# Kernel tuning notes

Measured on AMD Instinct MI355X. Metric: run time of the kernel, lower is better.

## Reference

```python
import jax, jax.numpy as jnp
import numpy as np

SF = 2  # shrink_factor


def resize_bilinear_ac(x, oh, ow):
    """Bilinear resize with align_corners=True, NCHW, matches torch F.interpolate."""
    B, C, H, W = x.shape
    if (oh, ow) == (H, W):
        return x
    ys = jnp.linspace(0.0, H - 1, oh)
    y0 = jnp.floor(ys).astype(jnp.int32)
    y1 = jnp.clip(y0 + 1, 0, H - 1)
    wy = (ys - y0).astype(x.dtype)
    xs = jnp.linspace(0.0, W - 1, ow)
    x0 = jnp.floor(xs).astype(jnp.int32)
    x1 = jnp.clip(x0 + 1, 0, W - 1)
    wx = (xs - x0).astype(x.dtype)
    t = x[:, :, y0, :] * (1 - wy)[None, None, :, None] + x[:, :, y1, :] * wy[None, None, :, None]
    return t[:, :, :, x0] * (1 - wx) + t[:, :, :, x1] * wx


def conv1x1(x, W, b):
    # x: [B,C,H,W], W: [O,C], b: [O]
    return jnp.einsum('bchw,oc->bohw', x, W) + b[None, :, None, None]


def setup_inputs() -> dict:
    key = jax.random.key(0)
    ks = jax.random.split(key, 8)
    B, C, H, W = 4, 512, 129, 129
    Cqk = C // 8
    s = 1.0 / np.sqrt(C)
    return {
        'x': jax.random.normal(ks[0], (B, C, H, W), jnp.float32),
        'Wq': jax.random.normal(ks[1], (Cqk, C), jnp.float32) * s,
        'bq': jax.random.normal(ks[2], (Cqk,), jnp.float32) * s,
        'Wk': jax.random.normal(ks[3], (Cqk, C), jnp.float32) * s,
        'bk': jax.random.normal(ks[4], (Cqk,), jnp.float32) * s,
        'Wv': jax.random.normal(ks[5], (C, C), jnp.float32) * s,
        'bv': jax.random.normal(ks[6], (C,), jnp.float32) * s,
        'gamma': jax.random.normal(ks[7], (1,), jnp.float32) * 0.1,
    }


def reference(x, Wq, bq, Wk, bk, Wv, bv, gamma):
    B, C, H, W = x.shape
    h = (H - 1) // SF + 1
    w = (W - 1) // SF + 1
    xs = resize_bilinear_ac(x, h, w)  # [B,C,h,w]
    N = h * w
    q = conv1x1(xs, Wq, bq).reshape(B, -1, N)  # [B,Cqk,N]
    k = conv1x1(xs, Wk, bk).reshape(B, -1, N)  # [B,Cqk,N]
    v = conv1x1(xs, Wv, bv).reshape(B, -1, N)  # [B,C,N]
    # energy[b,n,m] = <q[:,n], k[:,m]>
    energy = jnp.einsum('bcn,bcm->bnm', q, k)  # [B,N,N]
    attention = jax.nn.softmax(energy, axis=-1)
    # out[b,c,n] = sum_m v[b,c,m] * attention[b,n,m]  (bmm(value, attention^T))
    out = jnp.einsum('bcm,bnm->bcn', v, attention).reshape(B, C, h, w)
    Hu = (h - 1) * SF + 1
    Wu = (w - 1) * SF + 1
    out = resize_bilinear_ac(out, Hu, Wu)
    out = gamma[0] * out + x
    return out, energy
```

## Files before the change

### kernel.cpp

```cpp
#include <hip/hip_runtime.h>
#include <hip/hip_bf16.h>
#include <cstdint>

#define BB 4
#define CC 512
#define CQK 64
#define HH 129
#define WW 129
#define HS 65
#define WSZ 65
#define NN 4225
#define NP 4352
#define KPV 4288
#define OUTSZ 34080768
#define ESZ 17850625
#define PLANE 16641

typedef unsigned short u16;
typedef __attribute__((ext_vector_type(8))) __bf16 bfrag;
typedef __attribute__((ext_vector_type(4))) float f4v;

__device__ inline u16 f2bf(float f) {
    union { float f; unsigned int u; } v; v.f = f;
    unsigned int u = v.u;
    return (u16)((u + 0x7FFFu + ((u >> 16) & 1u)) >> 16);
}
__device__ inline float bf2f(u16 v) {
    union { unsigned u; float f; } x; x.u = (unsigned)v << 16; return x.f;
}

__device__ __forceinline__ void gload16(const u16* g, u16* l) {
    __builtin_amdgcn_global_load_lds(
        (const __attribute__((address_space(1))) void*)g,
        (__attribute__((address_space(3))) void*)l, 16, 0, 0);
}

__global__ __launch_bounds__(256) void setup_k(const float* __restrict__ Wq,
                                               const float* __restrict__ Wk,
                                               const float* __restrict__ Wv,
                                               const float* __restrict__ x,
                                               u16* __restrict__ Wc,
                                               u16* __restrict__ XsT) {
    __shared__ u16 tile[64][65];
    if (blockIdx.x < 1280) {
        int idx = blockIdx.x * 256 + threadIdx.x;
        int o = idx >> 9, c = idx & 511;
        float v = (o < 64) ? Wq[o * 512 + c] : (o < 128) ? Wk[(o - 64) * 512 + c] : Wv[(o - 128) * 512 + c];
        Wc[idx] = f2bf(v);
        return;
    }
    int bid = blockIdx.x - 1280;
    int nt = bid % 68;
    int ct = (bid / 68) & 7;
    int b = bid / 544;
    int t = threadIdx.x;
#pragma unroll
    for (int l = 0; l < 16; ++l) {
        int e = t + l * 256;
        int ci = e >> 6, nj = e & 63;
        int n = nt * 64 + nj;
        int nc = n < (NN - 1) ? n : (NN - 1);
        int i = nc / 65, j = nc % 65;
        int c = ct * 64 + ci;
        float v = x[(((size_t)b * CC + c) * HH + 2 * i) * WW + 2 * j];
        tile[ci][nj] = f2bf(v);
    }
    __syncthreads();
#pragma unroll
    for (int l = 0; l < 16; ++l) {
        int e = t + l * 256;
        int nj = e >> 6, ci = e & 63;
        XsT[((size_t)b * NP + nt * 64 + nj) * 512 + ct * 64 + ci] = tile[ci][nj];
    }
}

template <int MODE>
__global__ __launch_bounds__(256) void gemm_nt(const u16* __restrict__ Abase,
                                               const u16* __restrict__ Bbase,
                                               int K, int lda, int ldb,
                                               float* __restrict__ outF,
                                               u16* __restrict__ out1, u16* __restrict__ out2,
                                               const float* __restrict__ bq,
                                               const float* __restrict__ bk,
                                               const float* __restrict__ bv,
                                               float* __restrict__ psums) {
    __shared__ __align__(16) u16 S[16384];
    u16* As = S;
    u16* Bs = S + 8192;

    int z; size_t m0, n0; unsigned xsave = 0;
    if (MODE == 0) {
        unsigned flat = blockIdx.x;
        unsigned s = flat & 7u;
        unsigned k = flat >> 3;
        unsigned m = k % 5u;
        unsigned nl = k / 5u;
        z = (int)(s >> 1);
        m0 = (size_t)m * 128;
        n0 = ((size_t)(s & 1u) * 17u + nl) * 128;
    } else {
        z = blockIdx.z;
        m0 = (size_t)blockIdx.y * 128;
        n0 = (size_t)blockIdx.x * 128;
        xsave = blockIdx.x;
    }

    const u16* A; const u16* Bm;
    if (MODE == 0) { A = Abase;                          Bm = Bbase + (size_t)z * NP * 512; }
    if (MODE == 1) { A = Abase + (size_t)z * NP * 128;   Bm = Bbase + (size_t)z * NP * 128 + 64; }

    const u16* Ab = A + m0 * lda;
    const u16* Bb = Bm + n0 * ldb;

    const int tid = threadIdx.x;
    const int lane = tid & 63, w = tid >> 6;
    const int wr = w >> 1, wc = w & 1;
    const int frow = lane & 15, fk = (lane >> 4) * 8;

    f4v acc[4][4];
#pragma unroll
    for (int i = 0; i < 4; ++i)
#pragma unroll
        for (int j = 0; j < 4; ++j) acc[i][j] = (f4v){0.f, 0.f, 0.f, 0.f};

    for (int kt = 0; kt < K; kt += 64) {
        if (kt) __syncthreads();
#pragma unroll
        for (int it = 0; it < 4; ++it) {
            int cb = (it * 4 + w) * 64;
            int chunk = cb + lane;
            int r = chunk >> 3;
            int kc = (chunk & 7) << 3;
            gload16(Ab + (size_t)r * lda + kt + kc, &As[cb * 8]);
            gload16(Bb + (size_t)r * ldb + kt + kc, &Bs[cb * 8]);
        }
        __syncthreads();
#pragma unroll
        for (int ks = 0; ks < 2; ++ks) {
            bfrag af[4], bf[4];
#pragma unroll
            for (int i = 0; i < 4; ++i)
                af[i] = *(const bfrag*)&As[(wr * 64 + i * 16 + frow) * 64 + ks * 32 + fk];
#pragma unroll
            for (int j = 0; j < 4; ++j)
                bf[j] = *(const bfrag*)&Bs[(wc * 64 + j * 16 + frow) * 64 + ks * 32 + fk];
#pragma unroll
            for (int i = 0; i < 4; ++i)
#pragma unroll
                for (int j = 0; j < 4; ++j)
                    acc[i][j] = __builtin_amdgcn_mfma_f32_16x16x32_bf16(af[i], bf[j], acc[i][j], 0, 0, 0);
        }
    }

    const int rbase = (lane >> 4) * 4, cbase = lane & 15;

    if (MODE == 0) {
        u16* out1b = out1 + (size_t)z * NP * 128;
        u16* out2b = out2 + (size_t)z * 512 * NP;
#pragma unroll
        for (int i = 0; i < 4; ++i)
#pragma unroll
            for (int j = 0; j < 4; ++j) {
                size_t row0 = m0 + wr * 64 + i * 16 + rbase;
                size_t col = n0 + wc * 64 + j * 16 + cbase;
#pragma unroll
                for (int r = 0; r < 4; ++r) {
                    int o = (int)(row0 + r);
                    float bias = (o < 64) ? bq[o] : (o < 128) ? bk[o - 64] : bv[o - 128];
                    u16 bb = f2bf(acc[i][j][r] + bias);
                    if (o < 128) out1b[col * 128 + o] = bb;
                    else out2b[(size_t)(o - 128) * NP + col] = bb;
                }
            }
    } else {
        float* eb = outF + (size_t)z * ESZ;
        u16* Pb = out1 + (size_t)z * NP * NP;
        float psl[4][4];
#pragma unroll
        for (int i = 0; i < 4; ++i)
#pragma unroll
            for (int r = 0; r < 4; ++r) psl[i][r] = 0.f;

        __syncthreads();
#pragma unroll
        for (int i = 0; i < 4; ++i)
#pragma unroll
            for (int j = 0; j < 4; ++j) {
                int rl = wr * 64 + i * 16 + rbase;
                int cl = wc * 64 + j * 16 + cbase;
                size_t row0 = m0 + rl;
                size_t col = n0 + cl;
#pragma unroll
                for (int r = 0; r < 4; ++r) {
                    float v = acc[i][j][r];
                    size_t ro = row0 + r;
                    float pe = (col < NN) ? __expf(v) : 0.f;
                    if (ro < NN && col < NN) eb[ro * NN + col] = v;
                    S[(rl + r) * 128 + cl] = f2bf(pe);
                    psl[i][r] += pe;
                }
            }
        float* pbase = psums + ((size_t)z * 68 + xsave * 2 + wc) * NP;
#pragma unroll
        for (int i = 0; i < 4; ++i)
#pragma unroll
            for (int r = 0; r < 4; ++r) {
                float s = psl[i][r];
                s += __shfl_xor(s, 1);
                s += __shfl_xor(s, 2);
                s += __shfl_xor(s, 4);
                s += __shfl_xor(s, 8);
                if (cbase == 0)
                    pbase[m0 + wr * 64 + i * 16 + rbase + r] = s;
            }
        __syncthreads();
        u16* pb = Pb + m0 * NP + n0;
#pragma unroll
        for (int l = 0; l < 8; ++l) {
            int idx = tid + l * 256;
            int row = idx >> 4, c16 = idx & 15;
            *(int4*)(pb + (size_t)row * NP + c16 * 8) = *(const int4*)&S[row * 128 + c16 * 8];
        }
    }
}

__global__ __launch_bounds__(256) void reduce_sums(const float* __restrict__ psums,
                                                   float* __restrict__ invsum) {
    int idx = blockIdx.x * 256 + threadIdx.x;
    if (idx >= BB * NP) return;
    int b = idx / NP, n = idx % NP;
    const float* p = psums + (size_t)b * 68 * NP + n;
    float s = 0.f;
#pragma unroll
    for (int ct = 0; ct < 68; ++ct) s += p[(size_t)ct * NP];
    invsum[idx] = 1.f / s;
}

__global__ __launch_bounds__(256) void gemm_pv(const u16* __restrict__ Vb,
                                               const u16* __restrict__ P,
                                               u16* __restrict__ ctxp,
                                               const float* __restrict__ invsum) {
    __shared__ __align__(16) u16 S[16384];
    u16* As = S;
    u16* Bs = S + 8192;

    unsigned flat = blockIdx.x + 34u * (blockIdx.y + 4u * blockIdx.z);
    unsigned swz = (flat & 7u) * 136u + (flat >> 3);
    unsigned zs = swz / 136u;
    unsigned rem = swz - zs * 136u;
    unsigned xs = rem >> 2;
    unsigned ys = rem & 3u;
    const int b = (int)(zs >> 1), half = (int)(zs & 1);

    const u16* A = Vb + (size_t)b * 512 * NP;
    const u16* Bm = P + (size_t)b * NP * NP;
    const size_t m0 = (size_t)ys * 128;
    const size_t n0 = (size_t)xs * 128;
    const u16* Ab = A + m0 * NP;
    const u16* Bb = Bm + n0 * NP;
    const int kbeg = half ? 2176 : 0;
    const int kend = half ? KPV : 2176;

    const int tid = threadIdx.x;
    const int lane = tid & 63, w = tid >> 6;
    const int wr = w >> 1, wc = w & 1;
    const int frow = lane & 15, fk = (lane >> 4) * 8;

    f4v acc[4][4];
#pragma unroll
    for (int i = 0; i < 4; ++i)
#pragma unroll
        for (int j = 0; j < 4; ++j) acc[i][j] = (f4v){0.f, 0.f, 0.f, 0.f};

    for (int kt = kbeg; kt < kend; kt += 64) {
        if (kt != kbeg) __syncthreads();
#pragma unroll
        for (int it = 0; it < 4; ++it) {
            int cb = (it * 4 + w) * 64;
            int chunk = cb + lane;
            int r = chunk >> 3;
            int kc = (chunk & 7) << 3;
            gload16(Ab + (size_t)r * NP + kt + kc, &As[cb * 8]);
            gload16(Bb + (size_t)r * NP + kt + kc, &Bs[cb * 8]);
        }
        __syncthreads();
#pragma unroll
        for (int ks = 0; ks < 2; ++ks) {
            bfrag af[4], bf[4];
#pragma unroll
            for (int i = 0; i < 4; ++i)
                af[i] = *(const bfrag*)&As[(wr * 64 + i * 16 + frow) * 64 + ks * 32 + fk];
#pragma unroll
            for (int j = 0; j < 4; ++j)
                bf[j] = *(const bfrag*)&Bs[(wc * 64 + j * 16 + frow) * 64 + ks * 32 + fk];
#pragma unroll
            for (int i = 0; i < 4; ++i)
#pragma unroll
                for (int j = 0; j < 4; ++j)
                    acc[i][j] = __builtin_amdgcn_mfma_f32_16x16x32_bf16(af[i], bf[j], acc[i][j], 0, 0, 0);
        }
    }

    const int rbase = (lane >> 4) * 4, cbase = lane & 15;
    const float* isb = invsum + (size_t)b * NP;
    __syncthreads();
#pragma unroll
    for (int j = 0; j < 4; ++j) {
        int cl = wc * 64 + j * 16 + cbase;
        float inv = isb[n0 + cl];
#pragma unroll
        for (int i = 0; i < 4; ++i) {
            int rl = wr * 64 + i * 16 + rbase;
#pragma unroll
            for (int r = 0; r < 4; ++r)
                S[(rl + r) * 128 + cl] = f2bf(acc[i][j][r] * inv);
        }
    }
    __syncthreads();
    u16* cb = ctxp + ((size_t)(half * BB + b) * 512 + m0) * NP + n0;
#pragma unroll
    for (int l = 0; l < 8; ++l) {
        int idx = tid + l * 256;
        int row = idx >> 4, c16 = idx & 15;
        *(int4*)(cb + (size_t)row * NP + c16 * 8) = *(const int4*)&S[row * 128 + c16 * 8];
    }
}

#define SLICE ((size_t)BB * 512 * NP)
__global__ __launch_bounds__(256) void upsample_add(const u16* __restrict__ ctxp,
                                                    const float* __restrict__ x,
                                                    const float* __restrict__ gm,
                                                    float* __restrict__ out) {
    __shared__ float cs[66 * 66];
    const int bc = blockIdx.x;
    const u16* p0 = ctxp + (size_t)bc * NP;
    const u16* p1 = p0 + SLICE;
    const int t = threadIdx.x;

    for (int idx = t; idx < 4225; idx += 256) {
        int r = idx / 65, c = idx - r * 65;
        cs[r * 66 + c] = bf2f(p0[idx]) + bf2f(p1[idx]);
    }
    if (t < 66) cs[t * 66 + 65] = 0.f;
    if (t >= 128 && t < 193) cs[65 * 66 + (t - 128)] = 0.f;
    __syncthreads();

    const float g = gm[0];
    const float* xb = x + (size_t)bc * PLANE;
    float* ob = out + (size_t)bc * PLANE;
    for (int idx = t; idx < PLANE; idx += 256) {
        int yy = idx / 129, xx = idx - yy * 129;
        int i0 = yy >> 1, j0 = xx >> 1;
        float wy = 0.5f * (float)(yy & 1), wx = 0.5f * (float)(xx & 1);
        const float* c0 = &cs[i0 * 66 + j0];
        float c00 = c0[0], c01 = c0[1], c10 = c0[66], c11 = c0[67];
        float cx0 = c00 + wx * (c01 - c00);
        float cx1 = c10 + wx * (c11 - c10);
        ob[idx] = g * (cx0 + wy * (cx1 - cx0)) + xb[idx];
    }
}

#define SZ_WC    ((size_t)640 * 512 * 2)
#define OFF_XST  (SZ_WC)
#define SZ_XST   ((size_t)BB * NP * 512 * 2)
#define OFF_QKT  (OFF_XST + SZ_XST)
#define SZ_QKT   ((size_t)BB * NP * 128 * 2)
#define OFF_V    (OFF_QKT + SZ_QKT)
#define SZ_V     ((size_t)BB * 512 * NP * 2)
#define OFF_PS   (OFF_V + SZ_V)
#define SZ_PS    ((size_t)BB * 68 * NP * 4)
#define OFF_INV  (OFF_PS + SZ_PS)
#define SZ_INV   ((size_t)BB * NP * 4)
#define OFF_CTXP (OFF_INV + SZ_INV)
#define SZ_CTXP  ((size_t)2 * BB * 512 * NP * 2)
#define OFF_P    (OFF_CTXP + SZ_CTXP)

extern "C" void kernel_launch(void* const* d_in, const int* in_sizes, int n_in,
                              void* d_out, int out_size, void* d_ws, size_t ws_size,
                              hipStream_t stream) {
    const float* x  = (const float*)d_in[0];
    const float* Wq = (const float*)d_in[1];
    const float* bq = (const float*)d_in[2];
    const float* Wk = (const float*)d_in[3];
    const float* bk = (const float*)d_in[4];
    const float* Wv = (const float*)d_in[5];
    const float* bv = (const float*)d_in[6];
    const float* gm = (const float*)d_in[7];

    float* out = (float*)d_out;
    float* energy = out + (size_t)OUTSZ;

    char* ws = (char*)d_ws;
    u16* Wc    = (u16*)(ws);
    u16* XsT   = (u16*)(ws + OFF_XST);
    u16* qkT   = (u16*)(ws + OFF_QKT);
    u16* V     = (u16*)(ws + OFF_V);
    float* psums  = (float*)(ws + OFF_PS);
    float* invsum = (float*)(ws + OFF_INV);
    u16* ctxp  = (u16*)(ws + OFF_CTXP);
    u16* P     = (u16*)(ws + OFF_P);

    setup_k<<<3456, 256, 0, stream>>>(Wq, Wk, Wv, x, Wc, XsT);
    gemm_nt<0><<<680, 256, 0, stream>>>(Wc, XsT, 512, 512, 512,
                                        nullptr, qkT, V, bq, bk, bv, nullptr);
    gemm_nt<1><<<dim3(34, 34, BB), 256, 0, stream>>>(qkT, qkT, 64, 128, 128,
                                                     energy, P, nullptr, nullptr, nullptr, nullptr,
                                                     psums);
    reduce_sums<<<68, 256, 0, stream>>>(psums, invsum);
    gemm_pv<<<dim3(34, 4, 8), 256, 0, stream>>>(V, P, ctxp, invsum);
    upsample_add<<<2048, 256, 0, stream>>>(ctxp, x, gm, out);
}
```

Measured before the change: 420.3 us.

## Use 32x32 MFMA with XOR-swizzled LDS in PV GEMM, nontemporal energy stores

The value-times-attention GEMM moves from 16x16x32 to 32x32x16 bf16 MFMA tiles (2x2 per wave). It adds an XOR swizzle on the LDS layout of the A and B tiles, aiming for fewer fragment loads and fewer LDS bank conflicts. The energy matrix writes and the strided x reads in setup now use nontemporal hints so this streaming traffic is less likely to evict reused data from cache. The epilogue row/column mapping is rewritten to match the 32x32 accumulator layout, and an error there would produce wrong outputs.

```diff
diff --git a/kernel.cpp b/kernel.cpp
--- a/kernel.cpp
+++ b/kernel.cpp
@@ -19,6 +19,7 @@
 typedef unsigned short u16;
 typedef __attribute__((ext_vector_type(8))) __bf16 bfrag;
 typedef __attribute__((ext_vector_type(4))) float f4v;
+typedef __attribute__((ext_vector_type(16))) float f16v;
 
 __device__ inline u16 f2bf(float f) {
     union { float f; unsigned int u; } v; v.f = f;
@@ -62,7 +63,7 @@
         int nc = n < (NN - 1) ? n : (NN - 1);
         int i = nc / 65, j = nc % 65;
         int c = ct * 64 + ci;
-        float v = x[(((size_t)b * CC + c) * HH + 2 * i) * WW + 2 * j];
+        float v = __builtin_nontemporal_load(&x[(((size_t)b * CC + c) * HH + 2 * i) * WW + 2 * j]);
         tile[ci][nj] = f2bf(v);
     }
     __syncthreads();
@@ -195,7 +196,8 @@
                     float v = acc[i][j][r];
                     size_t ro = row0 + r;
                     float pe = (col < NN) ? __expf(v) : 0.f;
-                    if (ro < NN && col < NN) eb[ro * NN + col] = v;
+                    if (ro < NN && col < NN)
+                        __builtin_nontemporal_store(v, &eb[ro * NN + col]);
                     S[(rl + r) * 128 + cl] = f2bf(pe);
                     psl[i][r] += pe;
                 }
@@ -264,13 +266,16 @@
     const int tid = threadIdx.x;
     const int lane = tid & 63, w = tid >> 6;
     const int wr = w >> 1, wc = w & 1;
-    const int frow = lane & 15, fk = (lane >> 4) * 8;
-
-    f4v acc[4][4];
-#pragma unroll
-    for (int i = 0; i < 4; ++i)
-#pragma unroll
-        for (int j = 0; j < 4; ++j) acc[i][j] = (f4v){0.f, 0.f, 0.f, 0.f};
+    const int r32 = lane & 31;
+    const int khalf = lane >> 5;
+
+    f16v acc[2][2];
+#pragma unroll
+    for (int i = 0; i < 2; ++i)
+#pragma unroll
+        for (int j = 0; j < 2; ++j)
+#pragma unroll
+            for (int r = 0; r < 16; ++r) acc[i][j][r] = 0.f;
 
     for (int kt = kbeg; kt < kend; kt += 64) {
         if (kt != kbeg) __syncthreads();
@@ -279,41 +284,52 @@
             int cb = (it * 4 + w) * 64;
             int chunk = cb + lane;
             int r = chunk >> 3;
-            int kc = (chunk & 7) << 3;
-            gload16(Ab + (size_t)r * NP + kt + kc, &As[cb * 8]);
-            gload16(Bb + (size_t)r * NP + kt + kc, &Bs[cb * 8]);
+            int kcb = ((chunk & 7) ^ (r & 7)) << 4;
+            gload16(Ab + (size_t)r * NP + kt + (kcb >> 1), &As[cb * 8]);
+            gload16(Bb + (size_t)r * NP + kt + (kcb >> 1), &Bs[cb * 8]);
         }
         __syncthreads();
 #pragma unroll
-        for (int ks = 0; ks < 2; ++ks) {
-            bfrag af[4], bf[4];
-#pragma unroll
-            for (int i = 0; i < 4; ++i)
-                af[i] = *(const bfrag*)&As[(wr * 64 + i * 16 + frow) * 64 + ks * 32 + fk];
-#pragma unroll
-            for (int j = 0; j < 4; ++j)
-                bf[j] = *(const bfrag*)&Bs[(wc * 64 + j * 16 + frow) * 64 + ks * 32 + fk];
-#pragma unroll
-            for (int i = 0; i < 4; ++i)
-#pragma unroll
-                for (int j = 0; j < 4; ++j)
-                    acc[i][j] = __builtin_amdgcn_mfma_f32_16x16x32_bf16(af[i], bf[j], acc[i][j], 0, 0, 0);
-        }
-    }
-
-    const int rbase = (lane >> 4) * 4, cbase = lane & 15;
+        for (int ks = 0; ks < 4; ++ks) {
+            bfrag a0, a1, b0, b1;
+            {
+                int row = wr * 64 + r32;
+                int L = row * 128 + ks * 32 + khalf * 16;
+                a0 = *(const bfrag*)((const char*)As + (L ^ ((row & 7) << 4)));
+                row += 32;
+                L = row * 128 + ks * 32 + khalf * 16;
+                a1 = *(const bfrag*)((const char*)As + (L ^ ((row & 7) << 4)));
+            }
+            {
+                int row = wc * 64 + r32;
+                int L = row * 128 + ks * 32 + khalf * 16;
+                b0 = *(const bfrag*)((const char*)Bs + (L ^ ((row & 7) << 4)));
+                row += 32;
+                L = row * 128 + ks * 32 + khalf * 16;
+                b1 = *(const bfrag*)((const char*)Bs + (L ^ ((row & 7) << 4)));
+            }
+            acc[0][0] = __builtin_amdgcn_mfma_f32_32x32x16_bf16(a0, b0, acc[0][0], 0, 0, 0);
+            acc[0][1] = __builtin_amdgcn_mfma_f32_32x32x16_bf16(a0, b1, acc[0][1], 0, 0, 0);
+            acc[1][0] = __builtin_amdgcn_mfma_f32_32x32x16_bf16(a1, b0, acc[1][0], 0, 0, 0);
+            acc[1][1] = __builtin_amdgcn_mfma_f32_32x32x16_bf16(a1, b1, acc[1][1], 0, 0, 0);
+        }
+    }
+
+    const int rquad = khalf * 4;
     const float* isb = invsum + (size_t)b * NP;
     __syncthreads();
 #pragma unroll
-    for (int j = 0; j < 4; ++j) {
-        int cl = wc * 64 + j * 16 + cbase;
+    for (int j = 0; j < 2; ++j) {
+        int cl = wc * 64 + j * 32 + r32;
         float inv = isb[n0 + cl];
 #pragma unroll
-        for (int i = 0; i < 4; ++i) {
-            int rl = wr * 64 + i * 16 + rbase;
-#pragma unroll
-            for (int r = 0; r < 4; ++r)
-                S[(rl + r) * 128 + cl] = f2bf(acc[i][j][r] * inv);
+        for (int i = 0; i < 2; ++i) {
+#pragma unroll
+            for (int reg = 0; reg < 16; ++reg) {
+                int rowl = (reg & 3) + 8 * (reg >> 2) + rquad;
+                int rl = wr * 64 + i * 32 + rowl;
+                S[rl * 128 + cl] = f2bf(acc[i][j][reg] * inv);
+            }
         }
     }
     __syncthreads();
```

Result: slower. 532.5 us (+26.7%).
